# Optimization experiments

Hardware: AMD Instinct MI355X
Metric: run time of the kernel (lower is better)

## Reference

```python
import jax, jax.numpy as jnp
import numpy as np

B, T, D, E, K = 4, 1024, 512, 10, 2
H = 4 * D          # expert hidden
CITY, CE = 8, 32   # num cities, city embedding dim
LIN = D + CE + D // 4 + D // 4 + D // 8 + D // 8  # 928 router input dim


def setup_inputs() -> dict:
    key = jax.random.key(0)
    ks = jax.random.split(key, 16)
    s = 0.02  # init scale for weights
    return {
        "x": jax.random.normal(ks[0], (B, T, D), jnp.float32),
        "delta_t": jax.random.normal(ks[1], (B, T, D // 4), jnp.float32),
        "delta_dis": jax.random.normal(ks[2], (B, T, D // 4), jnp.float32),
        "delta_rg": jax.random.normal(ks[3], (B, T, D // 8), jnp.float32),
        "delta_entropy": jax.random.normal(ks[4], (B, T, D // 8), jnp.float32),
        "city_emb": jax.random.normal(ks[5], (CITY, CE), jnp.float32),
        "Wg": jax.random.normal(ks[6], (E, LIN), jnp.float32) * s,
        "bg": jnp.zeros((E,), jnp.float32),
        "Wn": jax.random.normal(ks[7], (E, LIN), jnp.float32) * s,
        "bn": jnp.zeros((E,), jnp.float32),
        "W1": jax.random.normal(ks[8], (E, D, H), jnp.float32) * s,
        "b1": jnp.zeros((E, H), jnp.float32),
        "W2": jax.random.normal(ks[9], (E, H, D), jnp.float32) * s,
        "b2": jnp.zeros((E, D), jnp.float32),
        "noise": jax.random.normal(ks[10], (B, T, E), jnp.float32),
        "city": jax.random.randint(ks[11], (B,), 0, CITY),
    }


def reference(x, delta_t, delta_dis, delta_rg, delta_entropy, city_emb,
              Wg, bg, Wn, bn, W1, b1, W2, b2, noise, city):
    # ---- router: concat features -> noisy top-k gating ----
    ce = city_emb[city]                                   # (B, CE)
    ce = jnp.broadcast_to(ce[:, None, :], (x.shape[0], x.shape[1], ce.shape[-1]))
    h = jnp.concatenate([x, ce, delta_t, delta_dis, delta_rg, delta_entropy], axis=-1)  # (B,T,LIN)
    logits = jnp.einsum('btl,el->bte', h, Wg) + bg        # clean gate logits
    gate1 = jax.nn.softmax(logits, axis=-1)               # dense gate (returned for aux loss)
    noise_logits = jnp.einsum('btl,el->bte', h, Wn) + bn
    noisy = logits + noise * jax.nn.softplus(noise_logits)
    _, idx = jax.lax.top_k(noisy, K)                      # (B,T,K)
    sel = jax.nn.one_hot(idx, E, dtype=noisy.dtype).sum(-2) > 0  # (B,T,E) bool
    gating = jax.nn.softmax(jnp.where(sel, noisy, -jnp.inf), axis=-1)  # zeros off top-k

    # ---- experts: dense compute, combine weighted by sparse gate ----
    flat_x = x.reshape(-1, D)                             # (N, D)
    flat_g = gating.reshape(-1, E)                        # (N, E), zero for non-selected
    hid = jax.nn.gelu(jnp.einsum('nd,edh->neh', flat_x, W1) + b1, approximate=False)
    y = jnp.einsum('neh,ehd->ned', hid, W2) + b2          # (N, E, D)
    out = jnp.einsum('ne,ned->nd', flat_g, y).reshape(x.shape)
    return out, gate1
```

## Files before the change

### kernel.cpp

```cpp
#include <hip/hip_runtime.h>
#include <hip/hip_bf16.h>

#define B_      4
#define T_      1024
#define NTOK    4096
#define D_      512
#define E_      10
#define H_      2048
#define LIN_    928
#define TOPK    2
#define BM      128
#define ROWS_CAP 9472
#define TILES_CAP 74

typedef __bf16 bf16x8 __attribute__((ext_vector_type(8)));
typedef float  f32x4  __attribute__((ext_vector_type(4)));
typedef unsigned short ushort8 __attribute__((ext_vector_type(8)));

#define OFF_W1T   0ull
#define SZ_W1T    (10ull*2048*512*2)
#define OFF_W2T   (OFF_W1T + SZ_W1T)
#define SZ_W2T    SZ_W1T
#define OFF_XG    (OFF_W2T + SZ_W2T)
#define SZ_XG     ((size_t)ROWS_CAP*512*2)
#define OFF_HID   (OFF_XG + SZ_XG)
#define SZ_HID    ((size_t)ROWS_CAP*2048*2)
#define OFF_Y     OFF_W1T
#define OFF_TOKE  (OFF_HID + SZ_HID)
#define OFF_TOKG  (OFF_TOKE + 32768)
#define OFF_TROWS (OFF_TOKG + 32768)
#define OFF_RANK  (OFF_TROWS + 32768)
#define OFF_CNT   (OFF_RANK + 32768)
#define OFF_OFFS  (OFF_CNT + 64)
#define OFF_TE    (OFF_OFFS + 64)
#define OFF_TR    (OFF_TE + 512)

static __device__ __forceinline__ unsigned short f2b(float f) {
  unsigned int u = __float_as_uint(f);
  unsigned int r = (u + 0x7fffu + ((u >> 16) & 1u)) >> 16;
  return (unsigned short)r;
}

static __device__ __forceinline__ void gld16(const void* g, void* l) {
  __builtin_amdgcn_global_load_lds(
      (const __attribute__((address_space(1))) unsigned int*)g,
      (__attribute__((address_space(3))) unsigned int*)l, 16, 0, 0);
}

struct WconvLds { float t[64][65]; };

static __device__ __forceinline__ void wconv_body(
    const float* __restrict__ src, unsigned short* __restrict__ dst,
    int R, int C, int e, int bx, int by, int tid, WconvLds* W) {
  int c0 = bx << 6, r0 = by << 6;
  int rr = tid >> 4, cc = (tid & 15) << 2;
  const float* s = src + ((size_t)e * R + r0 + rr) * C + c0 + cc;
#pragma unroll
  for (int p = 0; p < 4; p++) {
    float4 v = *(const float4*)(s + (size_t)p * 16 * C);
    W->t[rr + p * 16][cc + 0] = v.x; W->t[rr + p * 16][cc + 1] = v.y;
    W->t[rr + p * 16][cc + 2] = v.z; W->t[rr + p * 16][cc + 3] = v.w;
  }
  __syncthreads();
  int wc2 = tid >> 2;
  unsigned short* d = dst + ((size_t)e * C + c0 + wc2) * R + r0;
#pragma unroll
  for (int p = 0; p < 4; p++) {
    int rb = ((tid & 3) << 2) + (p << 4);
    ushort4 o;
    o.x = f2b(W->t[rb + 0][wc2]); o.y = f2b(W->t[rb + 1][wc2]);
    o.z = f2b(W->t[rb + 2][wc2]); o.w = f2b(W->t[rb + 3][wc2]);
    *(ushort4*)&d[rb] = o;
  }
}

__global__ __launch_bounds__(256) void prep_k(
    const float* __restrict__ x, const float* __restrict__ dt,
    const float* __restrict__ dd, const float* __restrict__ dr,
    const float* __restrict__ de, const float* __restrict__ cemb,
    const int* __restrict__ city,
    const float* __restrict__ Wg, const float* __restrict__ Wn,
    const float* __restrict__ W1, const float* __restrict__ W2,
    unsigned short* __restrict__ w1T, unsigned short* __restrict__ w2T,
    float* __restrict__ logits_all, int* __restrict__ counts) {
  __shared__ WconvLds W;
  int bx = blockIdx.x;
  int tid = threadIdx.x;
  if (bx >= 256) {
    int idx = bx - 256;
    if (idx < 2560) wconv_body(W1, w1T, 512, 2048, idx / 256, idx & 31, (idx >> 5) & 7, tid, &W);
    else { idx -= 2560; wconv_body(W2, w2T, 2048, 512, idx / 256, idx & 7, (idx >> 3) & 31, tid, &W); }
    return;
  }
  if (bx == 0 && tid < E_) counts[tid] = 0;
  int lane = tid & 63;
  int gw = bx * 4 + (tid >> 6);
  int n0 = gw * 4;
  int cb = city[n0 >> 10];

  float acc[4][20];
#pragma unroll
  for (int j = 0; j < 4; j++)
#pragma unroll
    for (int o = 0; o < 20; o++) acc[j][o] = 0.f;

  {
    float hce = (lane < 32) ? cemb[cb * 32 + lane] : 0.f;
    int c = 512 + (lane & 31);
#pragma unroll
    for (int o = 0; o < 10; o++) {
      float wg = Wg[o * LIN_ + c];
      float wn = Wn[o * LIN_ + c];
#pragma unroll
      for (int j = 0; j < 4; j++) {
        acc[j][o]      = fmaf(hce, wg, acc[j][o]);
        acc[j][10 + o] = fmaf(hce, wn, acc[j][10 + o]);
      }
    }
  }
#pragma unroll
  for (int s = 0; s < 5; s++) {
    const float* hp; int W2_, cofs;
    if      (s == 0) { hp = x;  W2_ = 512; cofs = 0;   }
    else if (s == 1) { hp = dt; W2_ = 128; cofs = 544; }
    else if (s == 2) { hp = dd; W2_ = 128; cofs = 672; }
    else if (s == 3) { hp = dr; W2_ = 64;  cofs = 800; }
    else             { hp = de; W2_ = 64;  cofs = 864; }
    for (int base = 0; base < W2_; base += 64) {
      int c = cofs + base + lane;
      float wv[20];
#pragma unroll
      for (int o = 0; o < 10; o++) {
        wv[o]      = Wg[o * LIN_ + c];
        wv[10 + o] = Wn[o * LIN_ + c];
      }
      float hv[4];
#pragma unroll
      for (int j = 0; j < 4; j++) hv[j] = hp[(size_t)(n0 + j) * W2_ + base + lane];
#pragma unroll
      for (int j = 0; j < 4; j++)
#pragma unroll
        for (int o = 0; o < 20; o++) acc[j][o] = fmaf(hv[j], wv[o], acc[j][o]);
    }
  }
#pragma unroll
  for (int off = 1; off < 64; off <<= 1) {
#pragma unroll
    for (int j = 0; j < 4; j++)
#pragma unroll
      for (int o = 0; o < 20; o++) acc[j][o] += __shfl_xor(acc[j][o], off);
  }
#pragma unroll
  for (int j = 0; j < 4; j++) {
    float v = 0.f;
#pragma unroll
    for (int o = 0; o < 20; o++) if (lane == o) v = acc[j][o];
    if (lane < 20) logits_all[(size_t)(n0 + j) * 20 + lane] = v;
  }
}

__global__ __launch_bounds__(256) void route2_k(
    const float* __restrict__ logits_all,
    const float* __restrict__ bg, const float* __restrict__ bn,
    const float* __restrict__ noise,
    float* __restrict__ gate1, int* __restrict__ tok_e,
    float* __restrict__ tok_g, int* __restrict__ ranks,
    int* __restrict__ counts) {
  __shared__ int lcnt[E_], lbase[E_];
  int tid = threadIdx.x;
  if (tid < E_) lcnt[tid] = 0;
  __syncthreads();
  int n = blockIdx.x * 256 + tid;
  const float* p = &logits_all[(size_t)n * 20];
  float logits[E_], noisy[E_], ex[E_];
  float mx = -3.4e38f;
#pragma unroll
  for (int e = 0; e < E_; e++) { logits[e] = p[e] + bg[e]; mx = fmaxf(mx, logits[e]); }
  float s = 0.f;
#pragma unroll
  for (int e = 0; e < E_; e++) { ex[e] = expf(logits[e] - mx); s += ex[e]; }
  float invs = 1.f / s;
#pragma unroll
  for (int e = 0; e < E_; e++) gate1[(size_t)n * E_ + e] = ex[e] * invs;
#pragma unroll
  for (int e = 0; e < E_; e++) {
    float t = p[10 + e] + bn[e];
    float sp = (t > 20.f) ? t : log1pf(expf(t));
    noisy[e] = logits[e] + noise[(size_t)n * E_ + e] * sp;
  }
  int i0 = 0; float v0 = noisy[0];
#pragma unroll
  for (int e = 1; e < E_; e++) if (noisy[e] > v0) { v0 = noisy[e]; i0 = e; }
  int i1 = -1; float v1 = -3.4e38f;
#pragma unroll
  for (int e = 0; e < E_; e++) if (e != i0 && noisy[e] > v1) { v1 = noisy[e]; i1 = e; }
  float ee = expf(v1 - v0);
  float g0 = 1.f / (1.f + ee);
  tok_e[2 * n] = i0; tok_e[2 * n + 1] = i1;
  tok_g[2 * n] = g0; tok_g[2 * n + 1] = ee * g0;
  int r0 = atomicAdd(&lcnt[i0], 1);
  int r1 = atomicAdd(&lcnt[i1], 1);
  __syncthreads();
  if (tid < E_) lbase[tid] = atomicAdd(&counts[tid], lcnt[tid]);
  __syncthreads();
  ranks[2 * n]     = lbase[i0] + r0;
  ranks[2 * n + 1] = lbase[i1] + r1;
}

__global__ void setup_k(const int* __restrict__ counts, int* __restrict__ offsets,
                        int* __restrict__ tile_e, int* __restrict__ tile_r0) {
  __shared__ int cnt[E_], pf[E_ + 1], tb[E_ + 1];
  int tid = threadIdx.x;
  if (tid < E_) cnt[tid] = counts[tid];
  __syncthreads();
  if (tid == 0) {
    int off = 0, tt = 0;
    for (int e = 0; e < E_; e++) {
      pf[e] = off; tb[e] = tt;
      int nt = (cnt[e] + BM - 1) / BM;
      tt += nt; off += nt * BM;
    }
    pf[E_] = off; tb[E_] = tt;
  }
  __syncthreads();
  if (tid < E_) offsets[tid] = pf[tid];
  if (tid == E_) offsets[E_] = pf[E_];
  if (tid < TILES_CAP) {
    int e = -1;
#pragma unroll
    for (int k = 0; k < E_; k++) if (tid >= tb[k] && tid < tb[k + 1]) e = k;
    if (e >= 0) { tile_e[tid] = e; tile_r0[tid] = pf[e] + (tid - tb[e]) * BM; }
    else        { tile_e[tid] = -1; tile_r0[tid] = 0; }
  }
}

__global__ __launch_bounds__(256) void scatgath_k(
    const float* __restrict__ x, const int* __restrict__ tok_e,
    const int* __restrict__ ranks, const int* __restrict__ offsets,
    int* __restrict__ token_rows, unsigned short* __restrict__ xg) {
  int n = blockIdx.x * 4 + (threadIdx.x >> 6);
  int lane = threadIdx.x & 63;
  int e0 = tok_e[2 * n], e1 = tok_e[2 * n + 1];
  int p0 = offsets[e0] + ranks[2 * n];
  int p1 = offsets[e1] + ranks[2 * n + 1];
  if (lane == 0) { token_rows[2 * n] = p0; token_rows[2 * n + 1] = p1; }
  float4 a = *(const float4*)&x[(size_t)n * D_ + lane * 8];
  float4 b = *(const float4*)&x[(size_t)n * D_ + lane * 8 + 4];
  ushort8 o;
  o[0] = f2b(a.x); o[1] = f2b(a.y); o[2] = f2b(a.z); o[3] = f2b(a.w);
  o[4] = f2b(b.x); o[5] = f2b(b.y); o[6] = f2b(b.z); o[7] = f2b(b.w);
  *(ushort8*)&xg[(size_t)p0 * D_ + lane * 8] = o;
  *(ushort8*)&xg[(size_t)p1 * D_ + lane * 8] = o;
}

template<int KD, int ND, int GX, int MODE>
__global__ __launch_bounds__(256) void gemm_k(
    const unsigned short* __restrict__ A, const unsigned short* __restrict__ BT,
    const float* __restrict__ bias, unsigned short* __restrict__ outb,
    float* __restrict__ outf,
    const int* __restrict__ tile_e, const int* __restrict__ tile_r0) {
  constexpr int BMT = 128, BNT = 128;
  constexpr int WN = BNT / 2;
  constexpr int FN = WN / 16;
  int nwg = GX * TILES_CAP;
  int fid = blockIdx.y * GX + blockIdx.x;
  int w = (fid & 7) * (nwg >> 3) + (fid >> 3);
  int bxs = w % GX, bys = w / GX;
  int e = tile_e[bys];
  if (e < 0) return;
  int row0 = tile_r0[bys];
  int n0 = bxs * BNT;
  int tid = threadIdx.x;
  int lane = tid & 63, wid = tid >> 6;
  int wr = wid >> 1, wc = wid & 1;
  __shared__ __align__(16) unsigned short LDS[2][(BMT + BNT) * 32];
  f32x4 acc[4][FN] = {};
  const unsigned short* Ab = A + (size_t)row0 * KD;
  const unsigned short* Bb = BT + ((size_t)e * ND + n0) * KD;
  int lrow = lane >> 2, lcol = (lane & 3) * 8;
  int r = lane & 15, g8 = (lane >> 4) * 8;

  auto stage = [&](int buf, int k0) {
#pragma unroll
    for (int i = 0; i < 4; i++) {
      int rowb = (wid + 4 * i) * 16;
      const unsigned short* src = (rowb < BMT)
          ? (Ab + (size_t)(rowb + lrow) * KD + k0 + lcol)
          : (Bb + (size_t)(rowb - BMT + lrow) * KD + k0 + lcol);
      gld16(src, &LDS[buf][rowb * 32]);
    }
  };

  stage(0, 0);
  __syncthreads();
  constexpr int NT = KD / 32;
  for (int t = 0; t < NT; t++) {
    int cur = t & 1;
    if (t + 1 < NT) stage(cur ^ 1, (t + 1) * 32);
    bf16x8 av[4], bv[FN];
#pragma unroll
    for (int mi = 0; mi < 4; mi++)
      av[mi] = *(const bf16x8*)&LDS[cur][(wr * 64 + mi * 16 + r) * 32 + g8];
#pragma unroll
    for (int ni = 0; ni < FN; ni++)
      bv[ni] = *(const bf16x8*)&LDS[cur][(BMT + wc * WN + ni * 16 + r) * 32 + g8];
#pragma unroll
    for (int mi = 0; mi < 4; mi++)
#pragma unroll
      for (int ni = 0; ni < FN; ni++)
        acc[mi][ni] = __builtin_amdgcn_mfma_f32_16x16x32_bf16(av[mi], bv[ni], acc[mi][ni], 0, 0, 0);
    __syncthreads();
  }
  int rq = (lane >> 4) * 4;
#pragma unroll
  for (int mi = 0; mi < 4; mi++) {
#pragma unroll
    for (int ni = 0; ni < FN; ni++) {
      int col = n0 + wc * WN + ni * 16 + r;
      float bz = (MODE == 0) ? bias[e * ND + col] : 0.f;
#pragma unroll
      for (int q = 0; q < 4; q++) {
        int row = row0 + wr * 64 + mi * 16 + rq + q;
        float v = acc[mi][ni][q];
        if constexpr (MODE == 0) {
          v += bz;
          v = 0.5f * v * (1.f + erff(v * 0.70710678118654752440f));
          outb[(size_t)row * ND + col] = f2b(v);
        } else {
          outf[(size_t)row * ND + col] = v;
        }
      }
    }
  }
}

__global__ void combine_k(const float* __restrict__ y, const float* __restrict__ b2,
                          const int* __restrict__ token_rows, const int* __restrict__ tok_e,
                          const float* __restrict__ tok_g, float* __restrict__ out) {
  int gid = blockIdx.x * 256 + threadIdx.x;
  int n = gid >> 7;
  int c = (gid & 127) << 2;
  int r0 = token_rows[2 * n], r1 = token_rows[2 * n + 1];
  int e0 = tok_e[2 * n], e1 = tok_e[2 * n + 1];
  float g0 = tok_g[2 * n], g1 = tok_g[2 * n + 1];
  float4 y0 = *(const float4*)&y[(size_t)r0 * D_ + c];
  float4 y1 = *(const float4*)&y[(size_t)r1 * D_ + c];
  float4 c0 = *(const float4*)&b2[e0 * D_ + c];
  float4 c1 = *(const float4*)&b2[e1 * D_ + c];
  float4 o;
  o.x = g0 * (y0.x + c0.x) + g1 * (y1.x + c1.x);
  o.y = g0 * (y0.y + c0.y) + g1 * (y1.y + c1.y);
  o.z = g0 * (y0.z + c0.z) + g1 * (y1.z + c1.z);
  o.w = g0 * (y0.w + c0.w) + g1 * (y1.w + c1.w);
  *(float4*)&out[(size_t)n * D_ + c] = o;
}

extern "C" void kernel_launch(void* const* d_in, const int* in_sizes, int n_in,
                              void* d_out, int out_size, void* d_ws, size_t ws_size,
                              hipStream_t stream) {
  const float* x     = (const float*)d_in[0];
  const float* dt    = (const float*)d_in[1];
  const float* dd    = (const float*)d_in[2];
  const float* dr    = (const float*)d_in[3];
  const float* de    = (const float*)d_in[4];
  const float* cemb  = (const float*)d_in[5];
  const float* Wg    = (const float*)d_in[6];
  const float* bg    = (const float*)d_in[7];
  const float* Wn    = (const float*)d_in[8];
  const float* bn    = (const float*)d_in[9];
  const float* W1    = (const float*)d_in[10];
  const float* b1    = (const float*)d_in[11];
  const float* W2    = (const float*)d_in[12];
  const float* b2    = (const float*)d_in[13];
  const float* noise = (const float*)d_in[14];
  const int*   city  = (const int*)d_in[15];

  float* out   = (float*)d_out;
  float* gate1 = out + (size_t)NTOK * D_;

  char* ws = (char*)d_ws;
  unsigned short* w1T = (unsigned short*)(ws + OFF_W1T);
  unsigned short* w2T = (unsigned short*)(ws + OFF_W2T);
  unsigned short* xg  = (unsigned short*)(ws + OFF_XG);
  unsigned short* hid = (unsigned short*)(ws + OFF_HID);
  float*  yb          = (float*)(ws + OFF_Y);
  int*    tok_e       = (int*)(ws + OFF_TOKE);
  float*  tok_g       = (float*)(ws + OFF_TOKG);
  int*    token_rows  = (int*)(ws + OFF_TROWS);
  int*    ranks       = (int*)(ws + OFF_RANK);
  int*    counts      = (int*)(ws + OFF_CNT);
  int*    offsets     = (int*)(ws + OFF_OFFS);
  int*    tile_e      = (int*)(ws + OFF_TE);
  int*    tile_r0     = (int*)(ws + OFF_TR);
  float*  logits_all  = (float*)(ws + OFF_HID);

  prep_k<<<5376, 256, 0, stream>>>(x, dt, dd, dr, de, cemb, city, Wg, Wn,
                                   W1, W2, w1T, w2T, logits_all, counts);
  route2_k<<<16, 256, 0, stream>>>(logits_all, bg, bn, noise, gate1, tok_e, tok_g,
                                   ranks, counts);
  setup_k<<<1, 256, 0, stream>>>(counts, offsets, tile_e, tile_r0);
  scatgath_k<<<1024, 256, 0, stream>>>(x, tok_e, ranks, offsets, token_rows, xg);
  gemm_k<512, 2048, 16, 0><<<dim3(16, TILES_CAP), 256, 0, stream>>>(xg, w1T, b1, hid, nullptr, tile_e, tile_r0);
  gemm_k<2048, 512, 4, 1><<<dim3(4, TILES_CAP), 256, 0, stream>>>(hid, w2T, nullptr, nullptr, yb, tile_e, tile_r0);
  combine_k<<<2048, 256, 0, stream>>>(yb, b2, token_rows, tok_e, tok_g, out);
}
```

Before: 123.6 us.

## Fuse routing into prep kernel, triple-buffer GEMM pipeline, store expert output in bf16

Routing (softmax, noisy top-2 gating, rank assignment) now runs inside the logit-reduction kernel, which removes the route2 launch and the logits_all round trip. The counts reset moves to a memset. The grouped GEMM goes from double to triple-buffered LDS with explicit vmcnt waits and raw barriers, so more loads are in flight while MFMAs run. The second GEMM writes bf16 instead of fp32 and combine reads 8 bf16 values per thread, halving that traffic at the cost of extra rounding on y.

```diff
diff --git a/kernel.cpp b/kernel.cpp
--- a/kernel.cpp
+++ b/kernel.cpp
@@ -41,6 +41,10 @@
   return (unsigned short)r;
 }
 
+static __device__ __forceinline__ float b2f(unsigned short u) {
+  return __uint_as_float(((unsigned int)u) << 16);
+}
+
 static __device__ __forceinline__ void gld16(const void* g, void* l) {
   __builtin_amdgcn_global_load_lds(
       (const __attribute__((address_space(1))) unsigned int*)g,
@@ -80,10 +84,15 @@
     const float* __restrict__ de, const float* __restrict__ cemb,
     const int* __restrict__ city,
     const float* __restrict__ Wg, const float* __restrict__ Wn,
+    const float* __restrict__ bg, const float* __restrict__ bn,
+    const float* __restrict__ noise,
     const float* __restrict__ W1, const float* __restrict__ W2,
     unsigned short* __restrict__ w1T, unsigned short* __restrict__ w2T,
-    float* __restrict__ logits_all, int* __restrict__ counts) {
+    float* __restrict__ gate1, int* __restrict__ tok_e,
+    float* __restrict__ tok_g, int* __restrict__ ranks,
+    int* __restrict__ counts) {
   __shared__ WconvLds W;
+  __shared__ int lcnt[E_], lbase[E_];
   int bx = blockIdx.x;
   int tid = threadIdx.x;
   if (bx >= 256) {
@@ -92,7 +101,8 @@
     else { idx -= 2560; wconv_body(W2, w2T, 2048, 512, idx / 256, idx & 7, (idx >> 3) & 31, tid, &W); }
     return;
   }
-  if (bx == 0 && tid < E_) counts[tid] = 0;
+  if (tid < E_) lcnt[tid] = 0;
+  __syncthreads();
   int lane = tid & 63;
   int gw = bx * 4 + (tid >> 6);
   int n0 = gw * 4;
@@ -120,13 +130,13 @@
   }
 #pragma unroll
   for (int s = 0; s < 5; s++) {
-    const float* hp; int W2_, cofs;
-    if      (s == 0) { hp = x;  W2_ = 512; cofs = 0;   }
-    else if (s == 1) { hp = dt; W2_ = 128; cofs = 544; }
-    else if (s == 2) { hp = dd; W2_ = 128; cofs = 672; }
-    else if (s == 3) { hp = dr; W2_ = 64;  cofs = 800; }
-    else             { hp = de; W2_ = 64;  cofs = 864; }
-    for (int base = 0; base < W2_; base += 64) {
+    const float* hp; int Wd, cofs;
+    if      (s == 0) { hp = x;  Wd = 512; cofs = 0;   }
+    else if (s == 1) { hp = dt; Wd = 128; cofs = 544; }
+    else if (s == 2) { hp = dd; Wd = 128; cofs = 672; }
+    else if (s == 3) { hp = dr; Wd = 64;  cofs = 800; }
+    else             { hp = de; Wd = 64;  cofs = 864; }
+    for (int base = 0; base < Wd; base += 64) {
       int c = cofs + base + lane;
       float wv[20];
 #pragma unroll
@@ -136,7 +146,7 @@
       }
       float hv[4];
 #pragma unroll
-      for (int j = 0; j < 4; j++) hv[j] = hp[(size_t)(n0 + j) * W2_ + base + lane];
+      for (int j = 0; j < 4; j++) hv[j] = hp[(size_t)(n0 + j) * Wd + base + lane];
 #pragma unroll
       for (int j = 0; j < 4; j++)
 #pragma unroll
@@ -150,61 +160,59 @@
 #pragma unroll
       for (int o = 0; o < 20; o++) acc[j][o] += __shfl_xor(acc[j][o], off);
   }
-#pragma unroll
-  for (int j = 0; j < 4; j++) {
-    float v = 0.f;
-#pragma unroll
-    for (int o = 0; o < 20; o++) if (lane == o) v = acc[j][o];
-    if (lane < 20) logits_all[(size_t)(n0 + j) * 20 + lane] = v;
-  }
-}
-
-__global__ __launch_bounds__(256) void route2_k(
-    const float* __restrict__ logits_all,
-    const float* __restrict__ bg, const float* __restrict__ bn,
-    const float* __restrict__ noise,
-    float* __restrict__ gate1, int* __restrict__ tok_e,
-    float* __restrict__ tok_g, int* __restrict__ ranks,
-    int* __restrict__ counts) {
-  __shared__ int lcnt[E_], lbase[E_];
-  int tid = threadIdx.x;
-  if (tid < E_) lcnt[tid] = 0;
-  __syncthreads();
-  int n = blockIdx.x * 256 + tid;
-  const float* p = &logits_all[(size_t)n * 20];
-  float logits[E_], noisy[E_], ex[E_];
-  float mx = -3.4e38f;
-#pragma unroll
-  for (int e = 0; e < E_; e++) { logits[e] = p[e] + bg[e]; mx = fmaxf(mx, logits[e]); }
-  float s = 0.f;
-#pragma unroll
-  for (int e = 0; e < E_; e++) { ex[e] = expf(logits[e] - mx); s += ex[e]; }
-  float invs = 1.f / s;
-#pragma unroll
-  for (int e = 0; e < E_; e++) gate1[(size_t)n * E_ + e] = ex[e] * invs;
-#pragma unroll
-  for (int e = 0; e < E_; e++) {
-    float t = p[10 + e] + bn[e];
-    float sp = (t > 20.f) ? t : log1pf(expf(t));
-    noisy[e] = logits[e] + noise[(size_t)n * E_ + e] * sp;
-  }
-  int i0 = 0; float v0 = noisy[0];
-#pragma unroll
-  for (int e = 1; e < E_; e++) if (noisy[e] > v0) { v0 = noisy[e]; i0 = e; }
-  int i1 = -1; float v1 = -3.4e38f;
-#pragma unroll
-  for (int e = 0; e < E_; e++) if (e != i0 && noisy[e] > v1) { v1 = noisy[e]; i1 = e; }
-  float ee = expf(v1 - v0);
-  float g0 = 1.f / (1.f + ee);
-  tok_e[2 * n] = i0; tok_e[2 * n + 1] = i1;
-  tok_g[2 * n] = g0; tok_g[2 * n + 1] = ee * g0;
-  int r0 = atomicAdd(&lcnt[i0], 1);
-  int r1 = atomicAdd(&lcnt[i1], 1);
+  float sv[20];
+#pragma unroll
+  for (int o = 0; o < 20; o++) {
+    float v = acc[0][o];
+    v = (lane == 1) ? acc[1][o] : v;
+    v = (lane == 2) ? acc[2][o] : v;
+    v = (lane == 3) ? acc[3][o] : v;
+    sv[o] = v;
+  }
+  int n = n0 + lane;
+  int i0 = 0, i1 = 0, rr0 = 0, rr1 = 0;
+  float gg0 = 0.f, gg1 = 0.f, gate[E_];
+#pragma unroll
+  for (int o = 0; o < E_; o++) gate[o] = 0.f;
+  if (lane < 4) {
+    float logits[E_], noisy[E_];
+    float mx = -3.4e38f;
+#pragma unroll
+    for (int o = 0; o < E_; o++) { logits[o] = sv[o] + bg[o]; mx = fmaxf(mx, logits[o]); }
+    float ssum = 0.f;
+#pragma unroll
+    for (int o = 0; o < E_; o++) { gate[o] = expf(logits[o] - mx); ssum += gate[o]; }
+    float inv = 1.f / ssum;
+#pragma unroll
+    for (int o = 0; o < E_; o++) gate[o] *= inv;
+#pragma unroll
+    for (int o = 0; o < E_; o++) {
+      float tt = sv[10 + o] + bn[o];
+      float sp = (tt > 20.f) ? tt : log1pf(expf(tt));
+      noisy[o] = logits[o] + noise[(size_t)n * E_ + o] * sp;
+    }
+    float v0 = noisy[0];
+#pragma unroll
+    for (int o = 1; o < E_; o++) if (noisy[o] > v0) { v0 = noisy[o]; i0 = o; }
+    float v1 = -3.4e38f; i1 = -1;
+#pragma unroll
+    for (int o = 0; o < E_; o++) if (o != i0 && noisy[o] > v1) { v1 = noisy[o]; i1 = o; }
+    float ee = expf(v1 - v0);
+    gg0 = 1.f / (1.f + ee); gg1 = ee * gg0;
+    rr0 = atomicAdd(&lcnt[i0], 1);
+    rr1 = atomicAdd(&lcnt[i1], 1);
+  }
   __syncthreads();
   if (tid < E_) lbase[tid] = atomicAdd(&counts[tid], lcnt[tid]);
   __syncthreads();
-  ranks[2 * n]     = lbase[i0] + r0;
-  ranks[2 * n + 1] = lbase[i1] + r1;
+  if (lane < 4) {
+    tok_e[2 * n] = i0;  tok_e[2 * n + 1] = i1;
+    tok_g[2 * n] = gg0; tok_g[2 * n + 1] = gg1;
+    ranks[2 * n]     = lbase[i0] + rr0;
+    ranks[2 * n + 1] = lbase[i1] + rr1;
+#pragma unroll
+    for (int o = 0; o < E_; o++) gate1[(size_t)n * E_ + o] = gate[o];
+  }
 }
 
 __global__ void setup_k(const int* __restrict__ counts, int* __restrict__ offsets,
@@ -257,11 +265,10 @@
 __global__ __launch_bounds__(256) void gemm_k(
     const unsigned short* __restrict__ A, const unsigned short* __restrict__ BT,
     const float* __restrict__ bias, unsigned short* __restrict__ outb,
-    float* __restrict__ outf,
     const int* __restrict__ tile_e, const int* __restrict__ tile_r0) {
   constexpr int BMT = 128, BNT = 128;
-  constexpr int WN = BNT / 2;
-  constexpr int FN = WN / 16;
+  constexpr int NT = KD / 32;
+  constexpr int BUFSZ = (BMT + BNT) * 32;
   int nwg = GX * TILES_CAP;
   int fid = blockIdx.y * GX + blockIdx.x;
   int w = (fid & 7) * (nwg >> 3) + (fid >> 3);
@@ -273,50 +280,61 @@
   int tid = threadIdx.x;
   int lane = tid & 63, wid = tid >> 6;
   int wr = wid >> 1, wc = wid & 1;
-  __shared__ __align__(16) unsigned short LDS[2][(BMT + BNT) * 32];
-  f32x4 acc[4][FN] = {};
+  __shared__ __align__(16) unsigned short LDS[3][BUFSZ];
+  f32x4 acc[4][4] = {};
   const unsigned short* Ab = A + (size_t)row0 * KD;
   const unsigned short* Bb = BT + ((size_t)e * ND + n0) * KD;
   int lrow = lane >> 2, lcol = (lane & 3) * 8;
   int r = lane & 15, g8 = (lane >> 4) * 8;
-
-  auto stage = [&](int buf, int k0) {
-#pragma unroll
-    for (int i = 0; i < 4; i++) {
-      int rowb = (wid + 4 * i) * 16;
-      const unsigned short* src = (rowb < BMT)
-          ? (Ab + (size_t)(rowb + lrow) * KD + k0 + lcol)
-          : (Bb + (size_t)(rowb - BMT + lrow) * KD + k0 + lcol);
-      gld16(src, &LDS[buf][rowb * 32]);
-    }
+  const unsigned short* gp[4];
+  int loff[4];
+#pragma unroll
+  for (int i = 0; i < 4; i++) {
+    int rowb = (wid + 4 * i) * 16;
+    gp[i] = (rowb < BMT) ? Ab + (size_t)(rowb + lrow) * KD + lcol
+                         : Bb + (size_t)(rowb - BMT + lrow) * KD + lcol;
+    loff[i] = rowb * 32;
+  }
+  auto stage = [&](int buf) {
+    unsigned short* lb = &LDS[0][0] + buf * BUFSZ;
+#pragma unroll
+    for (int i = 0; i < 4; i++) { gld16(gp[i], lb + loff[i]); gp[i] += 32; }
   };
-
-  stage(0, 0);
-  __syncthreads();
-  constexpr int NT = KD / 32;
-  for (int t = 0; t < NT; t++) {
-    int cur = t & 1;
-    if (t + 1 < NT) stage(cur ^ 1, (t + 1) * 32);
-    bf16x8 av[4], bv[FN];
+  stage(0); stage(1);
+  int cur = 0, nb = 2;
+  for (int t = 0; t < NT; ++t) {
+    if (t + 2 < NT) {
+      stage(nb);
+      asm volatile("s_waitcnt vmcnt(8)" ::: "memory");
+    } else if (t + 2 == NT) {
+      asm volatile("s_waitcnt vmcnt(4)" ::: "memory");
+    } else {
+      asm volatile("s_waitcnt vmcnt(0)" ::: "memory");
+    }
+    asm volatile("s_barrier" ::: "memory");
+    const unsigned short* cb2 = &LDS[0][0] + cur * BUFSZ;
+    bf16x8 av[4], bv[4];
 #pragma unroll
     for (int mi = 0; mi < 4; mi++)
-      av[mi] = *(const bf16x8*)&LDS[cur][(wr * 64 + mi * 16 + r) * 32 + g8];
-#pragma unroll
-    for (int ni = 0; ni < FN; ni++)
-      bv[ni] = *(const bf16x8*)&LDS[cur][(BMT + wc * WN + ni * 16 + r) * 32 + g8];
+      av[mi] = *(const bf16x8*)&cb2[(wr * 64 + mi * 16 + r) * 32 + g8];
+#pragma unroll
+    for (int ni = 0; ni < 4; ni++)
+      bv[ni] = *(const bf16x8*)&cb2[(BMT + wc * 64 + ni * 16 + r) * 32 + g8];
 #pragma unroll
     for (int mi = 0; mi < 4; mi++)
 #pragma unroll
-      for (int ni = 0; ni < FN; ni++)
+      for (int ni = 0; ni < 4; ni++)
         acc[mi][ni] = __builtin_amdgcn_mfma_f32_16x16x32_bf16(av[mi], bv[ni], acc[mi][ni], 0, 0, 0);
-    __syncthreads();
+    asm volatile("s_barrier" ::: "memory");
+    cur = (cur == 2) ? 0 : cur + 1;
+    nb = (nb == 2) ? 0 : nb + 1;
   }
   int rq = (lane >> 4) * 4;
 #pragma unroll
   for (int mi = 0; mi < 4; mi++) {
 #pragma unroll
-    for (int ni = 0; ni < FN; ni++) {
-      int col = n0 + wc * WN + ni * 16 + r;
+    for (int ni = 0; ni < 4; ni++) {
+      int col = n0 + wc * 64 + ni * 16 + r;
       float bz = (MODE == 0) ? bias[e * ND + col] : 0.f;
 #pragma unroll
       for (int q = 0; q < 4; q++) {
@@ -325,34 +343,34 @@
         if constexpr (MODE == 0) {
           v += bz;
           v = 0.5f * v * (1.f + erff(v * 0.70710678118654752440f));
-          outb[(size_t)row * ND + col] = f2b(v);
-        } else {
-          outf[(size_t)row * ND + col] = v;
         }
+        outb[(size_t)row * ND + col] = f2b(v);
       }
     }
   }
 }
 
-__global__ void combine_k(const float* __restrict__ y, const float* __restrict__ b2,
+__global__ void combine_k(const unsigned short* __restrict__ y, const float* __restrict__ b2,
                           const int* __restrict__ token_rows, const int* __restrict__ tok_e,
                           const float* __restrict__ tok_g, float* __restrict__ out) {
   int gid = blockIdx.x * 256 + threadIdx.x;
-  int n = gid >> 7;
-  int c = (gid & 127) << 2;
+  int n = gid >> 6;
+  int c = (gid & 63) << 3;
   int r0 = token_rows[2 * n], r1 = token_rows[2 * n + 1];
   int e0 = tok_e[2 * n], e1 = tok_e[2 * n + 1];
   float g0 = tok_g[2 * n], g1 = tok_g[2 * n + 1];
-  float4 y0 = *(const float4*)&y[(size_t)r0 * D_ + c];
-  float4 y1 = *(const float4*)&y[(size_t)r1 * D_ + c];
-  float4 c0 = *(const float4*)&b2[e0 * D_ + c];
-  float4 c1 = *(const float4*)&b2[e1 * D_ + c];
-  float4 o;
-  o.x = g0 * (y0.x + c0.x) + g1 * (y1.x + c1.x);
-  o.y = g0 * (y0.y + c0.y) + g1 * (y1.y + c1.y);
-  o.z = g0 * (y0.z + c0.z) + g1 * (y1.z + c1.z);
-  o.w = g0 * (y0.w + c0.w) + g1 * (y1.w + c1.w);
-  *(float4*)&out[(size_t)n * D_ + c] = o;
+  ushort8 y0 = *(const ushort8*)&y[(size_t)r0 * D_ + c];
+  ushort8 y1 = *(const ushort8*)&y[(size_t)r1 * D_ + c];
+  float ba[8], bb[8], o[8];
+  *(float4*)&ba[0] = *(const float4*)&b2[e0 * D_ + c];
+  *(float4*)&ba[4] = *(const float4*)&b2[e0 * D_ + c + 4];
+  *(float4*)&bb[0] = *(const float4*)&b2[e1 * D_ + c];
+  *(float4*)&bb[4] = *(const float4*)&b2[e1 * D_ + c + 4];
+#pragma unroll
+  for (int j = 0; j < 8; j++)
+    o[j] = g0 * (b2f(y0[j]) + ba[j]) + g1 * (b2f(y1[j]) + bb[j]);
+  *(float4*)&out[(size_t)n * D_ + c]     = *(float4*)&o[0];
+  *(float4*)&out[(size_t)n * D_ + c + 4] = *(float4*)&o[4];
 }
 
 extern "C" void kernel_launch(void* const* d_in, const int* in_sizes, int n_in,
@@ -379,11 +397,11 @@
   float* gate1 = out + (size_t)NTOK * D_;
 
   char* ws = (char*)d_ws;
-  unsigned short* w1T = (unsigned short*)(ws + OFF_W1T);
-  unsigned short* w2T = (unsigned short*)(ws + OFF_W2T);
-  unsigned short* xg  = (unsigned short*)(ws + OFF_XG);
-  unsigned short* hid = (unsigned short*)(ws + OFF_HID);
-  float*  yb          = (float*)(ws + OFF_Y);
+  unsigned short* w1T  = (unsigned short*)(ws + OFF_W1T);
+  unsigned short* w2T  = (unsigned short*)(ws + OFF_W2T);
+  unsigned short* xg   = (unsigned short*)(ws + OFF_XG);
+  unsigned short* hid  = (unsigned short*)(ws + OFF_HID);
+  unsigned short* yb16 = (unsigned short*)(ws + OFF_Y);
   int*    tok_e       = (int*)(ws + OFF_TOKE);
   float*  tok_g       = (float*)(ws + OFF_TOKG);
   int*    token_rows  = (int*)(ws + OFF_TROWS);
@@ -392,15 +410,14 @@
   int*    offsets     = (int*)(ws + OFF_OFFS);
   int*    tile_e      = (int*)(ws + OFF_TE);
   int*    tile_r0     = (int*)(ws + OFF_TR);
-  float*  logits_all  = (float*)(ws + OFF_HID);
-
-  prep_k<<<5376, 256, 0, stream>>>(x, dt, dd, dr, de, cemb, city, Wg, Wn,
-                                   W1, W2, w1T, w2T, logits_all, counts);
-  route2_k<<<16, 256, 0, stream>>>(logits_all, bg, bn, noise, gate1, tok_e, tok_g,
+
+  hipMemsetAsync(counts, 0, E_ * sizeof(int), stream);
+  prep_k<<<5376, 256, 0, stream>>>(x, dt, dd, dr, de, cemb, city, Wg, Wn, bg, bn,
+                                   noise, W1, W2, w1T, w2T, gate1, tok_e, tok_g,
                                    ranks, counts);
   setup_k<<<1, 256, 0, stream>>>(counts, offsets, tile_e, tile_r0);
   scatgath_k<<<1024, 256, 0, stream>>>(x, tok_e, ranks, offsets, token_rows, xg);
-  gemm_k<512, 2048, 16, 0><<<dim3(16, TILES_CAP), 256, 0, stream>>>(xg, w1T, b1, hid, nullptr, tile_e, tile_r0);
-  gemm_k<2048, 512, 4, 1><<<dim3(4, TILES_CAP), 256, 0, stream>>>(hid, w2T, nullptr, nullptr, yb, tile_e, tile_r0);
-  combine_k<<<2048, 256, 0, stream>>>(yb, b2, token_rows, tok_e, tok_g, out);
-}
+  gemm_k<512, 2048, 16, 0><<<dim3(16, TILES_CAP), 256, 0, stream>>>(xg, w1T, b1, hid, tile_e, tile_r0);
+  gemm_k<2048, 512, 4, 1><<<dim3(4, TILES_CAP), 256, 0, stream>>>(hid, w2T, nullptr, yb16, tile_e, tile_r0);
+  combine_k<<<1024, 256, 0, stream>>>(yb16, b2, token_rows, tok_e, tok_g, out);
+}
```

New measurement: 135.2 us. 9.4% more time.
